# Optimization experiments

Hardware: AMD Instinct MI355X
Metric: run time of the kernel (lower is better)

Reference implementation:

```python
import jax, jax.numpy as jnp
import numpy as np
import math

B, N, D, H = 4, 2048, 256, 4
DH = D // H
EPS = 1e-8


def setup_inputs() -> dict:
    key = jax.random.key(0)
    ks = jax.random.split(key, 8)
    x = jax.random.normal(ks[0], (B, N, D), dtype=jnp.float32)
    # RoPE rotation freqs: exp(i * pos * inv_freq), stored as (cos, sin) pairs -> [N, DH//2, 2]
    d2 = DH // 2
    inv_freq = 1.0 / (10000.0 ** (jnp.arange(d2, dtype=jnp.float32) / d2))
    ang = jnp.arange(N, dtype=jnp.float32)[:, None] * inv_freq[None, :]
    freqs = jnp.stack([jnp.cos(ang), jnp.sin(ang)], axis=-1)  # [N, d2, 2]
    s = 0.02
    g = jnp.ones((D,), dtype=jnp.float32)
    w_qkv = jax.random.normal(ks[1], (D, 3 * D), dtype=jnp.float32) * s
    b_qkv = jnp.zeros((3 * D,), dtype=jnp.float32)
    w_out = jax.random.normal(ks[2], (D, D), dtype=jnp.float32) * s
    b_out = jnp.zeros((D,), dtype=jnp.float32)
    w_gate = jax.random.normal(ks[3], (D, D), dtype=jnp.float32) * s
    b_gate = jnp.zeros((D,), dtype=jnp.float32)
    return {"x": x, "freqs": freqs, "g": g, "w_qkv": w_qkv, "b_qkv": b_qkv,
            "w_out": w_out, "b_out": b_out, "w_gate": w_gate, "b_gate": b_gate}


def _zcrmsnorm(x, g):
    x0 = x - jnp.mean(x, axis=-1, keepdims=True)
    rms = jnp.sqrt(jnp.mean(x0 * x0, axis=-1, keepdims=True) + EPS)
    return x0 / rms * g


def _rope(q, freqs):
    # q: [B,H,N,DH]; freqs: [N,DH//2,2] (cos,sin). Complex multiply on adjacent pairs.
    b, h, n, dh = q.shape
    qp = q.reshape(b, h, n, dh // 2, 2)
    cos = freqs[:n, :, 0][None, None]  # [1,1,N,d2]
    sin = freqs[:n, :, 1][None, None]
    q0, q1 = qp[..., 0], qp[..., 1]
    out = jnp.stack([q0 * cos - q1 * sin, q0 * sin + q1 * cos], axis=-1)
    return out.reshape(b, h, n, dh)


def reference(x, freqs, g, w_qkv, b_qkv, w_out, b_out, w_gate, b_gate):
    b, n, d = x.shape
    h = _zcrmsnorm(x, g)
    qkv = (h @ w_qkv + b_qkv).reshape(b, n, 3, H, DH)
    qkv = jnp.transpose(qkv, (2, 0, 3, 1, 4))  # [3,B,H,N,DH]
    q, k, v = qkv[0], qkv[1], qkv[2]
    q = _rope(q, freqs)
    k = _rope(k, freqs)
    scores = jnp.einsum('bhqd,bhkd->bhqk', q, k) / math.sqrt(DH)
    attn = jax.nn.softmax(scores, axis=-1)  # dropout is identity in eval
    y = jnp.einsum('bhqk,bhkd->bhqd', attn, v)
    y = jnp.transpose(y, (0, 2, 1, 3)).reshape(b, n, d)
    y = y @ w_out + b_out
    gate = jax.nn.sigmoid(h @ w_gate + b_gate)
    return x + gate * y
```

## Files before the change

### kernel.cpp

```cpp
#include <hip/hip_runtime.h>

typedef unsigned short u16;
typedef unsigned int u32;
typedef short short8 __attribute__((ext_vector_type(8)));
typedef float f32x4 __attribute__((ext_vector_type(4)));
typedef float f32x16 __attribute__((ext_vector_type(16)));

#define B_ 4
#define N_ 2048
#define D_ 256
#define H_ 4
#define DH_ 64
#define BN_ 8192

__device__ inline float b2f(u16 u) {
    union { u32 i; float f; } v; v.i = ((u32)u) << 16; return v.f;
}
__device__ inline u16 f2b(float f) {
    union { float f; u32 i; } v; v.f = f;
    return (u16)((v.i + 0x8000u) >> 16);
}
__device__ inline u32 pkbf(float a, float b) {
    union { float f; u32 i; } ua, ub; ua.f = a; ub.f = b;
    return __builtin_amdgcn_perm(ub.i + 0x8000u, ua.i + 0x8000u, 0x07060302u);
}
__device__ inline f32x4 mfma16(short8 a, short8 b, f32x4 c) {
    return __builtin_amdgcn_mfma_f32_16x16x32_bf16(a, b, c, 0, 0, 0);
}
__device__ inline f32x16 mfma32(short8 a, short8 b, f32x16 c) {
    return __builtin_amdgcn_mfma_f32_32x32x16_bf16(a, b, c, 0, 0, 0);
}

__device__ __forceinline__ void gemm_body(
    int bx, int by, int tid,
    const u16* __restrict__ A, const u16* __restrict__ BT,
    const float* __restrict__ bias, void* __restrict__ Cout,
    int Ntot)
{
    const int wave = tid >> 6, lane = tid & 63;
    const int ln15 = lane & 15, quad = lane >> 4;
    const int m0 = bx * 128 + (wave & 1) * 64;
    const int n0 = by * 128 + (wave >> 1) * 64;

    const f32x4 zero = {0.f, 0.f, 0.f, 0.f};
    f32x4 acc[4][4];
    #pragma unroll
    for (int i = 0; i < 4; ++i)
        #pragma unroll
        for (int j = 0; j < 4; ++j) acc[i][j] = zero;

    #pragma unroll
    for (int k0 = 0; k0 < 256; k0 += 32) {
        const int koff = k0 + quad * 8;
        short8 a[4], b[4];
        #pragma unroll
        for (int i = 0; i < 4; ++i)
            a[i] = *(const short8*)(A + (size_t)(m0 + i * 16 + ln15) * 256 + koff);
        #pragma unroll
        for (int j = 0; j < 4; ++j)
            b[j] = *(const short8*)(BT + (size_t)(n0 + j * 16 + ln15) * 256 + koff);
        #pragma unroll
        for (int i = 0; i < 4; ++i)
            #pragma unroll
            for (int j = 0; j < 4; ++j)
                acc[i][j] = mfma16(a[i], b[j], acc[i][j]);
    }

    #pragma unroll
    for (int i = 0; i < 4; ++i) {
        const int r = m0 + i * 16 + quad * 4;
        #pragma unroll
        for (int j = 0; j < 4; ++j) {
            const int c = n0 + j * 16 + ln15;
            const float bv = bias[c];
            #pragma unroll
            for (int rg = 0; rg < 4; ++rg) {
                const size_t idx = (size_t)(r + rg) * Ntot + c;
                ((u16*)Cout)[idx] = f2b(acc[i][j][rg] + bv);
            }
        }
    }
}

__device__ __forceinline__ void gemm_thin_body(
    int bx, int by, int tid,
    const u16* __restrict__ A, const u16* __restrict__ BT,
    const float* __restrict__ bias, void* __restrict__ Cout,
    const float* __restrict__ xin, const u16* __restrict__ gate,
    int mode)
{
    const int wave = tid >> 6, lane = tid & 63;
    const int ln15 = lane & 15, quad = lane >> 4;
    const int m0 = bx * 64 + (wave & 1) * 32;
    const int n0 = by * 64 + (wave >> 1) * 32;

    const f32x4 zero = {0.f, 0.f, 0.f, 0.f};
    f32x4 acc[2][2];
    #pragma unroll
    for (int i = 0; i < 2; ++i)
        #pragma unroll
        for (int j = 0; j < 2; ++j) acc[i][j] = zero;

    #pragma unroll
    for (int k0 = 0; k0 < 256; k0 += 32) {
        const int koff = k0 + quad * 8;
        short8 a[2], b[2];
        #pragma unroll
        for (int i = 0; i < 2; ++i)
            a[i] = *(const short8*)(A + (size_t)(m0 + i * 16 + ln15) * 256 + koff);
        #pragma unroll
        for (int j = 0; j < 2; ++j)
            b[j] = *(const short8*)(BT + (size_t)(n0 + j * 16 + ln15) * 256 + koff);
        #pragma unroll
        for (int i = 0; i < 2; ++i)
            #pragma unroll
            for (int j = 0; j < 2; ++j)
                acc[i][j] = mfma16(a[i], b[j], acc[i][j]);
    }

    #pragma unroll
    for (int i = 0; i < 2; ++i) {
        const int r = m0 + i * 16 + quad * 4;
        #pragma unroll
        for (int j = 0; j < 2; ++j) {
            const int c = n0 + j * 16 + ln15;
            const float bv = bias[c];
            #pragma unroll
            for (int rg = 0; rg < 4; ++rg) {
                const size_t idx = (size_t)(r + rg) * 256 + c;
                float v = acc[i][j][rg] + bv;
                if (mode == 1) {
                    ((u16*)Cout)[idx] = f2b(1.0f / (1.0f + __expf(-v)));
                } else {
                    ((float*)Cout)[idx] = xin[idx] + b2f(gate[idx]) * v;
                }
            }
        }
    }
}

__global__ __launch_bounds__(256) void gemm_ep(
    const u16* __restrict__ A, const u16* __restrict__ BT,
    const float* __restrict__ bias, void* __restrict__ Cout, int Ntot)
{
    gemm_body(blockIdx.x, blockIdx.y, threadIdx.x, A, BT, bias, Cout, Ntot);
}

__global__ __launch_bounds__(256) void gemm_thin(
    const u16* __restrict__ A, const u16* __restrict__ BT,
    const float* __restrict__ bias, void* __restrict__ Cout,
    const float* __restrict__ xin, const u16* __restrict__ gate, int mode)
{
    gemm_thin_body(blockIdx.x, blockIdx.y, threadIdx.x, A, BT, bias, Cout,
                   xin, gate, mode);
}

__global__ __launch_bounds__(256) void norm_transw_k(
    const float* __restrict__ x, const float* __restrict__ g, u16* __restrict__ h,
    const float* __restrict__ wqkv, const float* __restrict__ wout,
    const float* __restrict__ wgate,
    u16* __restrict__ wqkvT, u16* __restrict__ woutT, u16* __restrict__ wgateT)
{
    if (blockIdx.x < 2048) {
        const int wave = threadIdx.x >> 6, lane = threadIdx.x & 63;
        const int t = blockIdx.x * 4 + wave;
        const float4 u = *(const float4*)(x + (size_t)t * D_ + lane * 4);
        float s  = u.x + u.y + u.z + u.w;
        float s2 = u.x * u.x + u.y * u.y + u.z * u.z + u.w * u.w;
        #pragma unroll
        for (int m = 1; m < 64; m <<= 1) {
            s  += __shfl_xor(s, m);
            s2 += __shfl_xor(s2, m);
        }
        float mean = s * (1.0f / D_);
        float var  = s2 * (1.0f / D_) - mean * mean;
        float rinv = rsqrtf(var + 1e-8f);
        const float4 gv = *(const float4*)(g + lane * 4);
        uint2 o;
        o.x = pkbf((u.x - mean) * rinv * gv.x, (u.y - mean) * rinv * gv.y);
        o.y = pkbf((u.z - mean) * rinv * gv.z, (u.w - mean) * rinv * gv.w);
        *(uint2*)(h + (size_t)t * D_ + lane * 4) = o;
    } else {
        int idx = (blockIdx.x - 2048) * 256 + threadIdx.x;
        if (idx < 768 * 256) {
            int nn = idx >> 8, kk = idx & 255;
            wqkvT[idx] = f2b(wqkv[kk * 768 + nn]);
        }
        idx -= 768 * 256;
        if (idx >= 0 && idx < 256 * 256) {
            int nn = idx >> 8, kk = idx & 255;
            woutT[idx]  = f2b(wout[kk * 256 + nn]);
            wgateT[idx] = f2b(wgate[kk * 256 + nn]);
        }
    }
}

#define QSCALE 0.18033688f
__global__ __launch_bounds__(256) void rope_vt_gate_k(
    const u16* __restrict__ qkv, const float* __restrict__ freqs,
    u16* __restrict__ Q, u16* __restrict__ K, u16* __restrict__ VT,
    const u16* __restrict__ h, const u16* __restrict__ wgateT,
    const float* __restrict__ b_gate, u16* __restrict__ gatb)
{
    __shared__ __align__(16) u16 tile[64 * 65];
    const int blk = blockIdx.x;
    if (blk < 1024) {
        const int idx = blk * 256 + threadIdx.x;
        const int t = idx >> 5, rem = idx & 31;
        const int hh = rem >> 3, s8 = rem & 7;
        const int b = t >> 11, n = t & 2047;

        const float4 f0 = *(const float4*)(freqs + (size_t)n * 64 + s8 * 8);
        const float4 f1 = *(const float4*)(freqs + (size_t)n * 64 + s8 * 8 + 4);

        const u16* qp = qkv + (size_t)t * 768 + hh * 64 + s8 * 8;
        const uint4 qv = *(const uint4*)qp;
        const uint4 kv = *(const uint4*)(qp + 256);

        const size_t off = ((size_t)(b * H_ + hh) * N_ + n) * DH_ + s8 * 8;
        uint4 qo, ko;
        {
            float q0 = b2f((u16)(qv.x & 0xffff)), q1 = b2f((u16)(qv.x >> 16));
            float k0 = b2f((u16)(kv.x & 0xffff)), k1 = b2f((u16)(kv.x >> 16));
            qo.x = pkbf((q0 * f0.x - q1 * f0.y) * QSCALE, (q0 * f0.y + q1 * f0.x) * QSCALE);
            ko.x = pkbf(k0 * f0.x - k1 * f0.y, k0 * f0.y + k1 * f0.x);
        }
        {
            float q0 = b2f((u16)(qv.y & 0xffff)), q1 = b2f((u16)(qv.y >> 16));
            float k0 = b2f((u16)(kv.y & 0xffff)), k1 = b2f((u16)(kv.y >> 16));
            qo.y = pkbf((q0 * f0.z - q1 * f0.w) * QSCALE, (q0 * f0.w + q1 * f0.z) * QSCALE);
            ko.y = pkbf(k0 * f0.z - k1 * f0.w, k0 * f0.w + k1 * f0.z);
        }
        {
            float q0 = b2f((u16)(qv.z & 0xffff)), q1 = b2f((u16)(qv.z >> 16));
            float k0 = b2f((u16)(kv.z & 0xffff)), k1 = b2f((u16)(kv.z >> 16));
            qo.z = pkbf((q0 * f1.x - q1 * f1.y) * QSCALE, (q0 * f1.y + q1 * f1.x) * QSCALE);
            ko.z = pkbf(k0 * f1.x - k1 * f1.y, k0 * f1.y + k1 * f1.x);
        }
        {
            float q0 = b2f((u16)(qv.w & 0xffff)), q1 = b2f((u16)(qv.w >> 16));
            float k0 = b2f((u16)(kv.w & 0xffff)), k1 = b2f((u16)(kv.w >> 16));
            qo.w = pkbf((q0 * f1.z - q1 * f1.w) * QSCALE, (q0 * f1.w + q1 * f1.z) * QSCALE);
            ko.w = pkbf(k0 * f1.z - k1 * f1.w, k0 * f1.w + k1 * f1.z);
        }
        *(uint4*)(Q + off) = qo;
        *(uint4*)(K + off) = ko;
    } else if (blk < 1536) {
        const int id2 = blk - 1024;
        const int bh = id2 & 15;
        const int n0 = (id2 >> 4) * 64;
        const int b = bh >> 2, hh = bh & 3;
        #pragma unroll
        for (int rep = 0; rep < 16; ++rep) {
            int idx = rep * 256 + threadIdx.x;
            int nl = idx >> 6, dh = idx & 63;
            tile[dh * 65 + nl] = qkv[(size_t)(b * N_ + n0 + nl) * 768 + 512 + hh * 64 + dh];
        }
        __syncthreads();
        #pragma unroll
        for (int rep = 0; rep < 16; ++rep) {
            int idx = rep * 256 + threadIdx.x;
            int dh = idx >> 6, nl = idx & 63;
            VT[((size_t)bh * 64 + dh) * N_ + n0 + nl] = tile[dh * 65 + nl];
        }
    } else {
        const int id3 = blk - 1536;
        gemm_thin_body(id3 & 127, id3 >> 7, threadIdx.x, h, wgateT, b_gate,
                       (void*)gatb, (const float*)nullptr, (const u16*)nullptr, 1);
    }
}

__global__ __launch_bounds__(256, 4) void attn_k(
    const u16* __restrict__ Q, const u16* __restrict__ K,
    const u16* __restrict__ VT, float* __restrict__ Op,
    float* __restrict__ lvp)
{
    __shared__ __align__(16) u16 Ks[2][64][64];
    __shared__ __align__(16) u16 Vs[2][64][64];
    const int tid = threadIdx.x;
    const int wave = tid >> 6, lane = tid & 63;
    const int l31 = lane & 31, hi = lane >> 5;
    const int id = blockIdx.x;
    const int bh   = ((id & 7) << 1) | ((id >> 3) & 1);
    const int quar = (id >> 4) & 3;
    const int q0   = (id >> 6) * 128 + wave * 32;
    const int kt0  = quar * 512;

    const u16* Qh = Q + (size_t)bh * N_ * DH_;
    const u16* Kh = K + (size_t)bh * N_ * DH_;
    const u16* Vh = VT + (size_t)bh * DH_ * N_;

    short8 bq[4];
    #pragma unroll
    for (int kc = 0; kc < 4; ++kc)
        bq[kc] = *(const short8*)(Qh + (size_t)(q0 + l31) * DH_ + kc * 16 + hi * 8);

    f32x16 o0, o1;
    #pragma unroll
    for (int i = 0; i < 16; ++i) { o0[i] = 0.f; o1[i] = 0.f; }
    float lv = 0.f;

    const int srow = tid >> 2, sq4 = tid & 3;
    const int sw = srow & 7;
    const int wg0 = ((sq4) ^ sw) * 8;
    const int wg1 = ((sq4 + 4) ^ sw) * 8;
    const int rsw = l31 & 7;

    {
        uint4 k0 = *(const uint4*)(Kh + (size_t)(kt0 + srow) * DH_ + sq4 * 8);
        uint4 k1 = *(const uint4*)(Kh + (size_t)(kt0 + srow) * DH_ + (sq4 + 4) * 8);
        uint4 v0 = *(const uint4*)(Vh + (size_t)srow * N_ + kt0 + sq4 * 8);
        uint4 v1 = *(const uint4*)(Vh + (size_t)srow * N_ + kt0 + (sq4 + 4) * 8);
        *(uint4*)&Ks[0][srow][wg0] = k0;
        *(uint4*)&Ks[0][srow][wg1] = k1;
        *(uint4*)&Vs[0][srow][wg0] = v0;
        *(uint4*)&Vs[0][srow][wg1] = v1;
    }
    __syncthreads();

    int p = 0;
    for (int c = 0; c < 8; ++c) {
        const bool more = (c + 1 < 8);
        uint4 k0, k1, v0, v1;
        if (more) {
            const int ktn = kt0 + (c + 1) * 64;
            k0 = *(const uint4*)(Kh + (size_t)(ktn + srow) * DH_ + sq4 * 8);
            k1 = *(const uint4*)(Kh + (size_t)(ktn + srow) * DH_ + (sq4 + 4) * 8);
            v0 = *(const uint4*)(Vh + (size_t)srow * N_ + ktn + sq4 * 8);
            v1 = *(const uint4*)(Vh + (size_t)srow * N_ + ktn + (sq4 + 4) * 8);
        }

        #pragma unroll
        for (int g = 0; g < 2; ++g) {
            f32x16 st;
            #pragma unroll
            for (int i = 0; i < 16; ++i) st[i] = 0.f;
            #pragma unroll
            for (int kc = 0; kc < 4; ++kc) {
                const int gran = ((2 * kc + hi) ^ rsw) * 8;
                short8 ka = *(const short8*)&Ks[p][g * 32 + l31][gran];
                st = mfma32(ka, bq[kc], st);
            }
            #pragma unroll
            for (int r = 0; r < 16; ++r) {
                st[r] = exp2f(st[r]);
                lv += st[r];
            }
            #pragma unroll
            for (int kc2 = 0; kc2 < 2; ++kc2) {
                u32 X0, X1, Y0, Y1;
                asm("v_cvt_pk_bf16_f32 %0, %1, %2" : "=v"(X0) : "v"(st[8*kc2+0]), "v"(st[8*kc2+1]));
                asm("v_cvt_pk_bf16_f32 %0, %1, %2" : "=v"(X1) : "v"(st[8*kc2+2]), "v"(st[8*kc2+3]));
                asm("v_cvt_pk_bf16_f32 %0, %1, %2" : "=v"(Y0) : "v"(st[8*kc2+4]), "v"(st[8*kc2+5]));
                asm("v_cvt_pk_bf16_f32 %0, %1, %2" : "=v"(Y1) : "v"(st[8*kc2+6]), "v"(st[8*kc2+7]));
                asm("v_permlane32_swap_b32 %0, %1" : "+v"(X0), "+v"(Y0));
                asm("v_permlane32_swap_b32 %0, %1" : "+v"(X1), "+v"(Y1));
                union { u32 u[4]; short8 s; } bf;
                bf.u[0] = X0; bf.u[1] = X1; bf.u[2] = Y0; bf.u[3] = Y1;
                const int gran = ((2 * (2 * g + kc2) + hi) ^ rsw) * 8;
                short8 va0 = *(const short8*)&Vs[p][l31][gran];
                short8 va1 = *(const short8*)&Vs[p][32 + l31][gran];
                o0 = mfma32(va0, bf.s, o0);
                o1 = mfma32(va1, bf.s, o1);
            }
        }

        if (more) {
            *(uint4*)&Ks[p ^ 1][srow][wg0] = k0;
            *(uint4*)&Ks[p ^ 1][srow][wg1] = k1;
            *(uint4*)&Vs[p ^ 1][srow][wg0] = v0;
            *(uint4*)&Vs[p ^ 1][srow][wg1] = v1;
        }
        __syncthreads();
        p ^= 1;
    }

    lv += __shfl_xor(lv, 32);
    const size_t rowo = ((size_t)(quar * 16 + bh) * N_ + q0 + l31) * DH_;
    #pragma unroll
    for (int go = 0; go < 2; ++go) {
        #pragma unroll
        for (int rq = 0; rq < 4; ++rq) {
            float4 w4;
            if (go == 0) {
                w4.x = o0[rq*4+0]; w4.y = o0[rq*4+1]; w4.z = o0[rq*4+2]; w4.w = o0[rq*4+3];
            } else {
                w4.x = o1[rq*4+0]; w4.y = o1[rq*4+1]; w4.z = o1[rq*4+2]; w4.w = o1[rq*4+3];
            }
            *(float4*)(Op + rowo + go * 32 + 8 * rq + 4 * hi) = w4;
        }
    }
    if (hi == 0) lvp[(size_t)(quar * 16 + bh) * N_ + q0 + l31] = lv;
}

__global__ __launch_bounds__(256) void combine_k(
    const float* __restrict__ Op, const float* __restrict__ lvp,
    u16* __restrict__ yt)
{
    const int t = blockIdx.x * 256 + threadIdx.x;
    const int dh0 = (t & 7) * 8;
    const int q   = (t >> 3) & 2047;
    const int bh  = t >> 14;
    float a[8];
    #pragma unroll
    for (int i = 0; i < 8; ++i) a[i] = 0.f;
    float lsum = 0.f;
    #pragma unroll
    for (int pp = 0; pp < 4; ++pp) {
        const size_t o0 = ((size_t)(pp * 16 + bh) * N_ + q) * DH_ + dh0;
        const float4 u0 = *(const float4*)(Op + o0);
        const float4 u1 = *(const float4*)(Op + o0 + 4);
        a[0] += u0.x; a[1] += u0.y; a[2] += u0.z; a[3] += u0.w;
        a[4] += u1.x; a[5] += u1.y; a[6] += u1.z; a[7] += u1.w;
        lsum += lvp[(size_t)(pp * 16 + bh) * N_ + q];
    }
    const float rl = 1.0f / lsum;
    uint4 w;
    w.x = pkbf(a[0] * rl, a[1] * rl);
    w.y = pkbf(a[2] * rl, a[3] * rl);
    w.z = pkbf(a[4] * rl, a[5] * rl);
    w.w = pkbf(a[6] * rl, a[7] * rl);
    const int b = bh >> 2, h = bh & 3;
    *(uint4*)(yt + ((size_t)b * N_ + q) * D_ + h * 64 + dh0) = w;
}

extern "C" void kernel_launch(void* const* d_in, const int* in_sizes, int n_in,
                              void* d_out, int out_size, void* d_ws, size_t ws_size,
                              hipStream_t stream) {
    const float* x      = (const float*)d_in[0];
    const float* freqs  = (const float*)d_in[1];
    const float* g      = (const float*)d_in[2];
    const float* w_qkv  = (const float*)d_in[3];
    const float* b_qkv  = (const float*)d_in[4];
    const float* w_out  = (const float*)d_in[5];
    const float* b_out  = (const float*)d_in[6];
    const float* w_gate = (const float*)d_in[7];
    const float* b_gate = (const float*)d_in[8];
    float* out = (float*)d_out;

    char* ws = (char*)d_ws;
    size_t off = 0;
    auto carve = [&](size_t nelem) -> u16* {
        u16* p = (u16*)(ws + off);
        off += ((nelem * 2 + 255) / 256) * 256;
        return p;
    };
    u16* h      = carve((size_t)BN_ * D_);
    u16* qkv    = carve((size_t)BN_ * 768);
    u16* Qb     = carve((size_t)BN_ * D_);
    u16* Kb     = carve((size_t)BN_ * D_);
    u16* VT     = carve((size_t)BN_ * D_);
    u16* gatb   = carve((size_t)BN_ * D_);
    u16* wqkvT  = carve((size_t)768 * 256);
    u16* woutT  = carve((size_t)256 * 256);
    u16* wgateT = carve((size_t)256 * 256);
    float* Op  = (float*)carve((size_t)4 * 16 * N_ * DH_ * 2);
    float* lvp = (float*)carve((size_t)4 * 16 * N_ * 2);
    u16*   yt  = Qb;

    hipLaunchKernelGGL(norm_transw_k, dim3(3072), dim3(256), 0, stream,
                       x, g, h, w_qkv, w_out, w_gate, wqkvT, woutT, wgateT);
    hipLaunchKernelGGL(gemm_ep, dim3(BN_ / 128, 6), dim3(256), 0, stream,
                       h, wqkvT, b_qkv, (void*)qkv, 768);
    hipLaunchKernelGGL(rope_vt_gate_k, dim3(2048), dim3(256), 0, stream,
                       qkv, freqs, Qb, Kb, VT, h, wgateT, b_gate, gatb);
    hipLaunchKernelGGL(attn_k, dim3(1024), dim3(256), 0, stream,
                       Qb, Kb, VT, Op, lvp);
    hipLaunchKernelGGL(combine_k, dim3(1024), dim3(256), 0, stream,
                       Op, lvp, yt);
    hipLaunchKernelGGL(gemm_thin, dim3(128, 4), dim3(256), 0, stream,
                       yt, woutT, b_out, (void*)out, x, gatb, 2);
}
```

Before: 162.2 us.

## Fuse RoPE, V transpose and gate GEMM into QKV GEMM epilogue

The separate QKV GEMM and rope/VT/gate kernel are merged into one gemm_front kernel. wqkvT and wgateT are laid out contiguously so a single 8-column-block grid covers QKV and the gate projection. RoPE, Q scaling, V transposition and the gate sigmoid are applied in the epilogue directly from accumulators. This removes the qkv intermediate round-trip through memory and one launch. In exchange, the epilogue does scattered 2-byte stores with a per-element shuffle and freqs load, and the grid shrinks to 512 larger blocks.

Result: faster. 148.8 us (-8.3%).

```diff
diff --git a/kernel.cpp b/kernel.cpp
--- a/kernel.cpp
+++ b/kernel.cpp
@@ -31,15 +31,20 @@
     return __builtin_amdgcn_mfma_f32_32x32x16_bf16(a, b, c, 0, 0, 0);
 }
 
-__device__ __forceinline__ void gemm_body(
-    int bx, int by, int tid,
+#define QSCALE 0.18033688f
+
+__global__ __launch_bounds__(256) void gemm_front(
     const u16* __restrict__ A, const u16* __restrict__ BT,
-    const float* __restrict__ bias, void* __restrict__ Cout,
-    int Ntot)
+    const float* __restrict__ b_qkv, const float* __restrict__ b_gate,
+    const float* __restrict__ freqs,
+    u16* __restrict__ Qb, u16* __restrict__ Kb,
+    u16* __restrict__ VT, u16* __restrict__ gatb)
 {
+    const int tid = threadIdx.x;
     const int wave = tid >> 6, lane = tid & 63;
     const int ln15 = lane & 15, quad = lane >> 4;
-    const int m0 = bx * 128 + (wave & 1) * 64;
+    const int by = blockIdx.y;
+    const int m0 = blockIdx.x * 128 + (wave & 1) * 64;
     const int n0 = by * 128 + (wave >> 1) * 64;
 
     const f32x4 zero = {0.f, 0.f, 0.f, 0.f};
@@ -66,33 +71,80 @@
                 acc[i][j] = mfma16(a[i], b[j], acc[i][j]);
     }
 
-    #pragma unroll
-    for (int i = 0; i < 4; ++i) {
-        const int r = m0 + i * 16 + quad * 4;
+    if (by < 4) {
         #pragma unroll
         for (int j = 0; j < 4; ++j) {
-            const int c = n0 + j * 16 + ln15;
-            const float bv = bias[c];
-            #pragma unroll
-            for (int rg = 0; rg < 4; ++rg) {
-                const size_t idx = (size_t)(r + rg) * Ntot + c;
-                ((u16*)Cout)[idx] = f2b(acc[i][j][rg] + bv);
-            }
-        }
-    }
-}
-
-__device__ __forceinline__ void gemm_thin_body(
-    int bx, int by, int tid,
+            const int c  = n0 + j * 16 + ln15;
+            const int hh = (c >> 6) & 3;
+            const int dh = c & 63;
+            const int d2 = dh >> 1;
+            const bool isQ = (c < 256);
+            const bool ev  = ((dh & 1) == 0);
+            const float bv = b_qkv[c];
+            u16* dst = isQ ? Qb : Kb;
+            #pragma unroll
+            for (int i = 0; i < 4; ++i) {
+                const int r = m0 + i * 16 + quad * 4;
+                #pragma unroll
+                for (int rg = 0; rg < 4; ++rg) {
+                    const int t = r + rg;
+                    const int n = t & 2047, b = t >> 11;
+                    float v = acc[i][j][rg] + bv;
+                    float pv = __shfl_xor(v, 1);
+                    const float2 cs = *(const float2*)(freqs + (size_t)n * 64 + d2 * 2);
+                    float o = ev ? (v * cs.x - pv * cs.y)
+                                 : (pv * cs.y + v * cs.x);
+                    if (isQ) o *= QSCALE;
+                    dst[((size_t)(b * H_ + hh) * N_ + n) * DH_ + dh] = f2b(o);
+                }
+            }
+        }
+    } else if (by < 6) {
+        #pragma unroll
+        for (int j = 0; j < 4; ++j) {
+            const int c  = n0 + j * 16 + ln15;
+            const int hh = (c >> 6) & 3;
+            const int dh = c & 63;
+            const float bv = b_qkv[c];
+            #pragma unroll
+            for (int i = 0; i < 4; ++i) {
+                const int r = m0 + i * 16 + quad * 4;
+                const int n = r & 2047, b = r >> 11;
+                uint2 w;
+                w.x = pkbf(acc[i][j][0] + bv, acc[i][j][1] + bv);
+                w.y = pkbf(acc[i][j][2] + bv, acc[i][j][3] + bv);
+                *(uint2*)(VT + ((size_t)(b * H_ + hh) * DH_ + dh) * N_ + n) = w;
+            }
+        }
+    } else {
+        #pragma unroll
+        for (int j = 0; j < 4; ++j) {
+            const int c  = n0 + j * 16 + ln15;
+            const int cg = c - 768;
+            const float bv = b_gate[cg];
+            #pragma unroll
+            for (int i = 0; i < 4; ++i) {
+                const int r = m0 + i * 16 + quad * 4;
+                #pragma unroll
+                for (int rg = 0; rg < 4; ++rg) {
+                    float v = acc[i][j][rg] + bv;
+                    gatb[(size_t)(r + rg) * 256 + cg] = f2b(1.0f / (1.0f + __expf(-v)));
+                }
+            }
+        }
+    }
+}
+
+__global__ __launch_bounds__(256) void gemm_thin(
     const u16* __restrict__ A, const u16* __restrict__ BT,
-    const float* __restrict__ bias, void* __restrict__ Cout,
-    const float* __restrict__ xin, const u16* __restrict__ gate,
-    int mode)
+    const float* __restrict__ bias, float* __restrict__ out,
+    const float* __restrict__ xin, const u16* __restrict__ gate)
 {
+    const int tid = threadIdx.x;
     const int wave = tid >> 6, lane = tid & 63;
     const int ln15 = lane & 15, quad = lane >> 4;
-    const int m0 = bx * 64 + (wave & 1) * 32;
-    const int n0 = by * 64 + (wave >> 1) * 32;
+    const int m0 = blockIdx.x * 64 + (wave & 1) * 32;
+    const int n0 = blockIdx.y * 64 + (wave >> 1) * 32;
 
     const f32x4 zero = {0.f, 0.f, 0.f, 0.f};
     f32x4 acc[2][2];
@@ -128,31 +180,10 @@
             #pragma unroll
             for (int rg = 0; rg < 4; ++rg) {
                 const size_t idx = (size_t)(r + rg) * 256 + c;
-                float v = acc[i][j][rg] + bv;
-                if (mode == 1) {
-                    ((u16*)Cout)[idx] = f2b(1.0f / (1.0f + __expf(-v)));
-                } else {
-                    ((float*)Cout)[idx] = xin[idx] + b2f(gate[idx]) * v;
-                }
-            }
-        }
-    }
-}
-
-__global__ __launch_bounds__(256) void gemm_ep(
-    const u16* __restrict__ A, const u16* __restrict__ BT,
-    const float* __restrict__ bias, void* __restrict__ Cout, int Ntot)
-{
-    gemm_body(blockIdx.x, blockIdx.y, threadIdx.x, A, BT, bias, Cout, Ntot);
-}
-
-__global__ __launch_bounds__(256) void gemm_thin(
-    const u16* __restrict__ A, const u16* __restrict__ BT,
-    const float* __restrict__ bias, void* __restrict__ Cout,
-    const float* __restrict__ xin, const u16* __restrict__ gate, int mode)
-{
-    gemm_thin_body(blockIdx.x, blockIdx.y, threadIdx.x, A, BT, bias, Cout,
-                   xin, gate, mode);
+                out[idx] = xin[idx] + b2f(gate[idx]) * (acc[i][j][rg] + bv);
+            }
+        }
+    }
 }
 
 __global__ __launch_bounds__(256) void norm_transw_k(
@@ -192,81 +223,6 @@
             woutT[idx]  = f2b(wout[kk * 256 + nn]);
             wgateT[idx] = f2b(wgate[kk * 256 + nn]);
         }
-    }
-}
-
-#define QSCALE 0.18033688f
-__global__ __launch_bounds__(256) void rope_vt_gate_k(
-    const u16* __restrict__ qkv, const float* __restrict__ freqs,
-    u16* __restrict__ Q, u16* __restrict__ K, u16* __restrict__ VT,
-    const u16* __restrict__ h, const u16* __restrict__ wgateT,
-    const float* __restrict__ b_gate, u16* __restrict__ gatb)
-{
-    __shared__ __align__(16) u16 tile[64 * 65];
-    const int blk = blockIdx.x;
-    if (blk < 1024) {
-        const int idx = blk * 256 + threadIdx.x;
-        const int t = idx >> 5, rem = idx & 31;
-        const int hh = rem >> 3, s8 = rem & 7;
-        const int b = t >> 11, n = t & 2047;
-
-        const float4 f0 = *(const float4*)(freqs + (size_t)n * 64 + s8 * 8);
-        const float4 f1 = *(const float4*)(freqs + (size_t)n * 64 + s8 * 8 + 4);
-
-        const u16* qp = qkv + (size_t)t * 768 + hh * 64 + s8 * 8;
-        const uint4 qv = *(const uint4*)qp;
-        const uint4 kv = *(const uint4*)(qp + 256);
-
-        const size_t off = ((size_t)(b * H_ + hh) * N_ + n) * DH_ + s8 * 8;
-        uint4 qo, ko;
-        {
-            float q0 = b2f((u16)(qv.x & 0xffff)), q1 = b2f((u16)(qv.x >> 16));
-            float k0 = b2f((u16)(kv.x & 0xffff)), k1 = b2f((u16)(kv.x >> 16));
-            qo.x = pkbf((q0 * f0.x - q1 * f0.y) * QSCALE, (q0 * f0.y + q1 * f0.x) * QSCALE);
-            ko.x = pkbf(k0 * f0.x - k1 * f0.y, k0 * f0.y + k1 * f0.x);
-        }
-        {
-            float q0 = b2f((u16)(qv.y & 0xffff)), q1 = b2f((u16)(qv.y >> 16));
-            float k0 = b2f((u16)(kv.y & 0xffff)), k1 = b2f((u16)(kv.y >> 16));
-            qo.y = pkbf((q0 * f0.z - q1 * f0.w) * QSCALE, (q0 * f0.w + q1 * f0.z) * QSCALE);
-            ko.y = pkbf(k0 * f0.z - k1 * f0.w, k0 * f0.w + k1 * f0.z);
-        }
-        {
-            float q0 = b2f((u16)(qv.z & 0xffff)), q1 = b2f((u16)(qv.z >> 16));
-            float k0 = b2f((u16)(kv.z & 0xffff)), k1 = b2f((u16)(kv.z >> 16));
-            qo.z = pkbf((q0 * f1.x - q1 * f1.y) * QSCALE, (q0 * f1.y + q1 * f1.x) * QSCALE);
-            ko.z = pkbf(k0 * f1.x - k1 * f1.y, k0 * f1.y + k1 * f1.x);
-        }
-        {
-            float q0 = b2f((u16)(qv.w & 0xffff)), q1 = b2f((u16)(qv.w >> 16));
-            float k0 = b2f((u16)(kv.w & 0xffff)), k1 = b2f((u16)(kv.w >> 16));
-            qo.w = pkbf((q0 * f1.z - q1 * f1.w) * QSCALE, (q0 * f1.w + q1 * f1.z) * QSCALE);
-            ko.w = pkbf(k0 * f1.z - k1 * f1.w, k0 * f1.w + k1 * f1.z);
-        }
-        *(uint4*)(Q + off) = qo;
-        *(uint4*)(K + off) = ko;
-    } else if (blk < 1536) {
-        const int id2 = blk - 1024;
-        const int bh = id2 & 15;
-        const int n0 = (id2 >> 4) * 64;
-        const int b = bh >> 2, hh = bh & 3;
-        #pragma unroll
-        for (int rep = 0; rep < 16; ++rep) {
-            int idx = rep * 256 + threadIdx.x;
-            int nl = idx >> 6, dh = idx & 63;
-            tile[dh * 65 + nl] = qkv[(size_t)(b * N_ + n0 + nl) * 768 + 512 + hh * 64 + dh];
-        }
-        __syncthreads();
-        #pragma unroll
-        for (int rep = 0; rep < 16; ++rep) {
-            int idx = rep * 256 + threadIdx.x;
-            int dh = idx >> 6, nl = idx & 63;
-            VT[((size_t)bh * 64 + dh) * N_ + n0 + nl] = tile[dh * 65 + nl];
-        }
-    } else {
-        const int id3 = blk - 1536;
-        gemm_thin_body(id3 & 127, id3 >> 7, threadIdx.x, h, wgateT, b_gate,
-                       (void*)gatb, (const float*)nullptr, (const u16*)nullptr, 1);
     }
 }
 
@@ -446,28 +402,25 @@
         return p;
     };
     u16* h      = carve((size_t)BN_ * D_);
-    u16* qkv    = carve((size_t)BN_ * 768);
     u16* Qb     = carve((size_t)BN_ * D_);
     u16* Kb     = carve((size_t)BN_ * D_);
     u16* VT     = carve((size_t)BN_ * D_);
     u16* gatb   = carve((size_t)BN_ * D_);
     u16* wqkvT  = carve((size_t)768 * 256);
+    u16* wgateT = carve((size_t)256 * 256);
     u16* woutT  = carve((size_t)256 * 256);
-    u16* wgateT = carve((size_t)256 * 256);
     float* Op  = (float*)carve((size_t)4 * 16 * N_ * DH_ * 2);
     float* lvp = (float*)carve((size_t)4 * 16 * N_ * 2);
     u16*   yt  = Qb;
 
     hipLaunchKernelGGL(norm_transw_k, dim3(3072), dim3(256), 0, stream,
                        x, g, h, w_qkv, w_out, w_gate, wqkvT, woutT, wgateT);
-    hipLaunchKernelGGL(gemm_ep, dim3(BN_ / 128, 6), dim3(256), 0, stream,
-                       h, wqkvT, b_qkv, (void*)qkv, 768);
-    hipLaunchKernelGGL(rope_vt_gate_k, dim3(2048), dim3(256), 0, stream,
-                       qkv, freqs, Qb, Kb, VT, h, wgateT, b_gate, gatb);
+    hipLaunchKernelGGL(gemm_front, dim3(64, 8), dim3(256), 0, stream,
+                       h, wqkvT, b_qkv, b_gate, freqs, Qb, Kb, VT, gatb);
     hipLaunchKernelGGL(attn_k, dim3(1024), dim3(256), 0, stream,
                        Qb, Kb, VT, Op, lvp);
     hipLaunchKernelGGL(combine_k, dim3(1024), dim3(256), 0, stream,
                        Op, lvp, yt);
     hipLaunchKernelGGL(gemm_thin, dim3(128, 4), dim3(256), 0, stream,
-                       yt, woutT, b_out, (void*)out, x, gatb, 2);
-}
+                       yt, woutT, b_out, out, x, gatb);
+}
```
